# Optimization experiments

Hardware: AMD Instinct MI355X
Metric: run time of the kernel (lower is better)

## Reference

```python
import jax, jax.numpy as jnp
import numpy as np

N = 100_000   # nodes
E = 3_200_000 # edges
K = 3         # num_stacks
T = 4         # num_layers (shared weights)
H = 16        # hidden channels of conv1
EPS = 1e-5    # BatchNorm eps


def setup_inputs() -> dict:
    key = jax.random.key(0)
    ks = jax.random.split(key, 12)
    def glorot(k, shape):
        fan = shape[-2] + shape[-1]
        return jax.random.normal(k, shape, jnp.float32) * (2.0 / fan) ** 0.5
    return {
        "x": jax.random.normal(ks[0], (N, 1), jnp.float32),
        "edge_index": jax.random.randint(ks[1], (2, E), 0, N, jnp.int32),
        "edge_weight": jax.random.uniform(ks[2], (E,), jnp.float32),
        # conv1: in=1, out=16  (init_weight [K,Fin,Fout], shared weight [K,Fout,Fout], root [K,Fin,Fout], bias [K,Fout])
        "conv1_init_w": glorot(ks[3], (K, 1, H)),
        "conv1_w": glorot(ks[4], (K, H, H)),
        "conv1_root_w": glorot(ks[5], (K, 1, H)),
        "conv1_bias": jnp.zeros((K, H), jnp.float32),
        # BatchNorm1d(16) in eval mode: running stats + affine params
        "bn1_gamma": jnp.ones((H,), jnp.float32),
        "bn1_beta": jnp.zeros((H,), jnp.float32),
        "bn1_mean": jnp.zeros((H,), jnp.float32),
        "bn1_var": jnp.ones((H,), jnp.float32),
        # conv2: in=16, out=1, act=None
        "conv2_init_w": glorot(ks[6], (K, H, 1)),
        "conv2_w": glorot(ks[7], (K, 1, 1)),
        "conv2_root_w": glorot(ks[8], (K, H, 1)),
        "conv2_bias": jnp.zeros((K, 1), jnp.float32),
    }


def _gcn_norm(edge_index, edge_weight):
    # ARMAConv uses gcn_norm with add_self_loops=False
    row, col = edge_index[0], edge_index[1]
    deg = jax.ops.segment_sum(edge_weight, col, num_segments=N)
    dis = jnp.where(deg > 0, jax.lax.rsqrt(jnp.maximum(deg, 1e-12)), 0.0)
    norm = dis[row] * edge_weight * dis[col]
    return row, col, norm


def _arma(x, row, col, norm, init_w, w, root_w, bias, act):
    # x: [N, Fin]; out per stack: [K, N, Fout]
    root = jnp.einsum('nf,kfo->kno', x, root_w) + bias[:, None, :]
    out = jnp.einsum('nf,kfo->kno', x, init_w)
    for t in range(T):
        if t > 0:
            out = jnp.einsum('kno,kop->knp', out, w)  # shared weight
        msg = out[:, row, :] * norm[None, :, None]     # [K, E, F] gather + scale
        out = jax.ops.segment_sum(msg.transpose(1, 0, 2), col, num_segments=N)  # [N, K, F]
        out = out.transpose(1, 0, 2) + root            # scatter-add + skip (root)
        if act:
            out = jax.nn.relu(out)
    return out.mean(axis=0)  # mean over stacks -> [N, Fout]


def reference(x, edge_index, edge_weight,
              conv1_init_w, conv1_w, conv1_root_w, conv1_bias,
              bn1_gamma, bn1_beta, bn1_mean, bn1_var,
              conv2_init_w, conv2_w, conv2_root_w, conv2_bias):
    row, col, norm = _gcn_norm(edge_index, edge_weight)
    h = _arma(x, row, col, norm, conv1_init_w, conv1_w, conv1_root_w, conv1_bias, act=True)
    # BatchNorm1d (eval) + ReLU; dropout is identity in eval
    h = (h - bn1_mean) * jax.lax.rsqrt(bn1_var + EPS) * bn1_gamma + bn1_beta
    h = jax.nn.relu(h)
    h = _arma(h, row, col, norm, conv2_init_w, conv2_w, conv2_root_w, conv2_bias, act=False)
    return jax.nn.sigmoid(h)  # [N, 1]
```

## Files before the change

### kernel.cpp

```cpp
#include <hip/hip_runtime.h>
#include <math.h>

#define NN 100000
#define NE 3200000
#define NBUCK 782
#define EPB 4096
#define NBLK 782
#define SB_Q 16
#define SCAP 4608
#define BN_EPS 1e-5f

static inline size_t alignup(size_t v) { return (v + 255) & ~size_t(255); }

__device__ inline unsigned short f2bf(float x) {
  unsigned u = __float_as_uint(x);
  u += 0x7FFF + ((u >> 16) & 1);
  return (unsigned short)(u >> 16);
}
__device__ inline float bf2f(unsigned short h) {
  return __uint_as_float((unsigned)h << 16);
}
__device__ inline float edgew(int e) {
  return __uint_as_float((unsigned)e & 0xFFFE0000u);
}

__global__ void k_hist(const int* __restrict__ col, int* __restrict__ cntm) {
  __shared__ int cnt[NBUCK];
  for (int i = threadIdx.x; i < NBUCK; i += 256) cnt[i] = 0;
  __syncthreads();
  int e0 = blockIdx.x * EPB;
  int nE = min(EPB, NE - e0);
  for (int i = threadIdx.x; i < nE; i += 256) atomicAdd(&cnt[col[e0 + i] >> 7], 1);
  __syncthreads();
  int* dst = cntm + (size_t)blockIdx.x * NBUCK;
  for (int i = threadIdx.x; i < NBUCK; i += 256) dst[i] = cnt[i];
}

__global__ void k_scanb(const int* __restrict__ cntm, int* __restrict__ basem,
                        int* __restrict__ btot) {
  __shared__ int s[NBLK][SB_Q + 1];
  int q0 = blockIdx.x * SB_Q;
  int nq = min(SB_Q, NBUCK - q0);
  int t = threadIdx.x;
  for (int idx = t; idx < NBLK * SB_Q; idx += 256) {
    int i = idx >> 4, j = idx & 15;
    s[i][j] = (j < nq) ? cntm[(size_t)i * NBUCK + q0 + j] : 0;
  }
  __syncthreads();
  int wave = t >> 6, lane = t & 63;
  for (int j = wave; j < SB_Q; j += 4) {
    int carry = 0;
    for (int c = 0; c < (NBLK + 63) / 64; ++c) {
      int i = c * 64 + lane;
      int v = (i < NBLK) ? s[i][j] : 0;
      int x = v;
      #pragma unroll
      for (int d = 1; d < 64; d <<= 1) {
        int tt = __shfl_up(x, d, 64);
        if (lane >= d) x += tt;
      }
      if (i < NBLK) s[i][j] = x - v + carry;
      carry += __shfl(x, 63, 64);
    }
    if (lane == 0 && j < nq) {
      btot[q0 + j] = carry;
      basem[(size_t)NBLK * NBUCK + q0 + j] = carry;
    }
  }
  __syncthreads();
  for (int idx = t; idx < NBLK * SB_Q; idx += 256) {
    int i = idx >> 4, j = idx & 15;
    if (j < nq) basem[(size_t)i * NBUCK + q0 + j] = s[i][j];
  }
}

__global__ void k_scanq(const int* __restrict__ btot, int* __restrict__ gbase) {
  __shared__ int s[NBUCK];
  __shared__ int c[256];
  const int NCH = (NBUCK + 3) / 4;
  int t = threadIdx.x;
  for (int i = t; i < NBUCK; i += 256) s[i] = btot[i];
  __syncthreads();
  if (t < NCH) {
    int b0 = 4 * t, sum = 0;
    #pragma unroll
    for (int j = 0; j < 4; ++j) if (b0 + j < NBUCK) sum += s[b0 + j];
    c[t] = sum;
  }
  __syncthreads();
  for (int d = 1; d < NCH; d <<= 1) {
    int v = (t < NCH && t >= d) ? c[t - d] : 0;
    __syncthreads();
    if (t < NCH) c[t] += v;
    __syncthreads();
  }
  if (t < NCH) {
    int b0 = 4 * t;
    int run = (t > 0) ? c[t - 1] : 0;
    #pragma unroll
    for (int j = 0; j < 4; ++j)
      if (b0 + j < NBUCK) { int v = s[b0 + j]; s[b0 + j] = run; run += v; }
  }
  __syncthreads();
  for (int i = t; i < NBUCK; i += 256) gbase[i] = s[i];
}

__global__ void k_scat(const int* __restrict__ row, const int* __restrict__ col,
                       const float* __restrict__ ew, const int* __restrict__ basem,
                       const int* __restrict__ gbase, int2* __restrict__ bin) {
  __shared__ int segB[NBUCK];
  __shared__ int cnt[NBUCK];
  __shared__ int csc[256];
  __shared__ int2 stage[EPB];
  __shared__ unsigned short qarr[EPB];
  int b = blockIdx.x, t = threadIdx.x;
  const int* rowA = basem + (size_t)b * NBUCK;
  const int* rowB = basem + (size_t)(b + 1) * NBUCK;
  for (int i = t; i < NBUCK; i += 256) {
    int a = rowA[i];
    segB[i] = gbase[i] + a;
    cnt[i] = rowB[i] - a;
  }
  __syncthreads();
  const int NCH = (NBUCK + 3) / 4;
  int q4 = 4 * t;
  if (t < NCH) {
    int sum = 0;
    #pragma unroll
    for (int j = 0; j < 4; ++j) if (q4 + j < NBUCK) sum += cnt[q4 + j];
    csc[t] = sum;
  }
  __syncthreads();
  for (int d = 1; d < NCH; d <<= 1) {
    int v = (t < NCH && t >= d) ? csc[t - d] : 0;
    __syncthreads();
    if (t < NCH) csc[t] += v;
    __syncthreads();
  }
  if (t < NCH) {
    int run = (t > 0) ? csc[t - 1] : 0;
    #pragma unroll
    for (int j = 0; j < 4; ++j)
      if (q4 + j < NBUCK) {
        int v = cnt[q4 + j];
        segB[q4 + j] -= run;
        cnt[q4 + j] = run;
        run += v;
      }
  }
  __syncthreads();
  int e0 = b * EPB;
  int nE = min(EPB, NE - e0);
  for (int i = t; i < nE; i += 256) {
    int e = e0 + i;
    int cc = col[e], q = cc >> 7;
    int p = atomicAdd(&cnt[q], 1);
    stage[p] = make_int2(row[e] | ((cc & 127) << 17), __float_as_int(ew[e]));
    qarr[p] = (unsigned short)q;
  }
  __syncthreads();
  for (int p = t; p < nE; p += 256) {
    int q = qarr[p];
    bin[segB[q] + p] = stage[p];
  }
}

__global__ void k_build(const int* __restrict__ gbase, const int* __restrict__ btot,
                        const int2* __restrict__ bin,
                        int* __restrict__ csr, float* __restrict__ dis,
                        int* __restrict__ nstart, int* __restrict__ ncnt) {
  __shared__ int2 stage[SCAP];
  __shared__ int cnt[128];
  __shared__ float degw[128];
  __shared__ int off[129];
  int b = blockIdx.x;
  int gb0 = gbase[b];
  int nb = btot[b];
  const int2* gb = bin + gb0;
  for (int i = threadIdx.x; i < 128; i += 256) { cnt[i] = 0; degw[i] = 0.f; }
  __syncthreads();
  for (int i = threadIdx.x; i < nb; i += 256) {
    int2 v = gb[i];
    if (i < SCAP) stage[i] = v;
    int c = (v.x >> 17) & 127;
    atomicAdd(&cnt[c], 1);
    atomicAdd(&degw[c], __int_as_float(v.y));
  }
  __syncthreads();
  if (threadIdx.x == 0) {
    int s = 0;
    for (int c = 0; c < 128; ++c) { off[c] = s; s += cnt[c]; }
    off[128] = s;
  }
  __syncthreads();
  for (int c = threadIdx.x; c < 128; c += 256) {
    int n = b * 128 + c;
    if (n < NN) {
      nstart[n] = gb0 + off[c];
      ncnt[n] = cnt[c];
      float d = degw[c];
      dis[n] = (d > 0.f) ? rsqrtf(fmaxf(d, 1e-12f)) : 0.f;
    }
  }
  __syncthreads();
  for (int i = threadIdx.x; i < 128; i += 256) cnt[i] = 0;
  __syncthreads();
  int* cb = csr + gb0;
  for (int i = threadIdx.x; i < nb; i += 256) {
    int2 v = (i < SCAP) ? stage[i] : gb[i];
    int c = (v.x >> 17) & 127;
    int pos = off[c] + atomicAdd(&cnt[c], 1);
    unsigned u = (unsigned)v.y;
    u += 0xFFFFu + ((u >> 17) & 1);
    cb[pos] = (v.x & 0x1FFFF) | (int)(u & 0xFFFE0000u);
  }
}

__global__ void k_init1(const float* __restrict__ x, const float* __restrict__ rw,
                        const float* __restrict__ bias, const float* __restrict__ dis,
                        unsigned short* __restrict__ root1, float* __restrict__ s) {
  int idx = blockIdx.x * 256 + threadIdx.x;
  if (idx >= NN * 16) return;
  int n = idx >> 4, f = idx & 15;
  float xv = x[n];
  if (f == 0) s[n] = dis[n] * xv;
  root1[n * 48 + f]      = f2bf(xv * rw[f]      + bias[f]);
  root1[n * 48 + 16 + f] = f2bf(xv * rw[16 + f] + bias[16 + f]);
  root1[n * 48 + 32 + f] = f2bf(xv * rw[32 + f] + bias[32 + f]);
}

__global__ void k_prop_first(const float* __restrict__ s,
                             const unsigned short* __restrict__ root,
                             ushort4* __restrict__ outp, const int* __restrict__ csr,
                             const int* __restrict__ nstart, const int* __restrict__ ncnt,
                             const float* __restrict__ dis, const float* __restrict__ w,
                             const float* __restrict__ iw) {
  __shared__ float ws[768];
  for (int i = threadIdx.x; i < 768; i += 256) ws[i] = w[i];
  __syncthreads();
  int f = threadIdx.x & 15;
  int n = (blockIdx.x * 256 + threadIdx.x) >> 4;
  if (n >= NN) return;
  int e0 = nstart[n], cnt = ncnt[n];
  float g = 0.f;
  for (int i = f; i < cnt; i += 16) {
    int e = csr[e0 + i];
    g = fmaf(edgew(e), s[e & 0x1FFFF], g);
  }
  #pragma unroll
  for (int d = 8; d; d >>= 1) g += __shfl_xor(g, d, 16);
  float dn = dis[n];
  float dg = dn * g;
  float a0 = fmaxf(fmaf(dg, iw[f],      bf2f(root[n * 48 + f])),      0.f);
  float a1 = fmaxf(fmaf(dg, iw[16 + f], bf2f(root[n * 48 + 16 + f])), 0.f);
  float a2 = fmaxf(fmaf(dg, iw[32 + f], bf2f(root[n * 48 + 32 + f])), 0.f);
  float n0 = 0.f, n1 = 0.f, n2 = 0.f;
  #pragma unroll
  for (int f2 = 0; f2 < 16; ++f2) {
    float b0 = __shfl(a0, f2, 16);
    float b1 = __shfl(a1, f2, 16);
    float b2v = __shfl(a2, f2, 16);
    n0 = fmaf(b0, ws[f2 * 16 + f], n0);
    n1 = fmaf(b1, ws[256 + f2 * 16 + f], n1);
    n2 = fmaf(b2v, ws[512 + f2 * 16 + f], n2);
  }
  ushort4 pk;
  pk.x = f2bf(dn * n0); pk.y = f2bf(dn * n1); pk.z = f2bf(dn * n2); pk.w = 0;
  outp[(size_t)n * 16 + f] = pk;
}

template <bool APPLY_W>
__global__ __launch_bounds__(256, 6)
void k_prop16(const ushort4* __restrict__ in,
              const unsigned short* __restrict__ root,
              ushort4* __restrict__ outp, const int* __restrict__ csr,
              const int* __restrict__ nstart, const int* __restrict__ ncnt,
              const float* __restrict__ dis, const float* __restrict__ w,
              const float* __restrict__ bng, const float* __restrict__ bnb,
              const float* __restrict__ bnm, const float* __restrict__ bnv,
              const float* __restrict__ iw2, const float* __restrict__ rw2,
              const float* __restrict__ b2,
              float4* __restrict__ root2, ushort4* __restrict__ o2) {
  __shared__ float ws[768];
  if (APPLY_W) {
    for (int i = threadIdx.x; i < 768; i += 256) ws[i] = w[i];
    __syncthreads();
  }
  int f = threadIdx.x & 15;
  int n = (blockIdx.x * 256 + threadIdx.x) >> 4;
  if (n >= NN) return;
  int e0 = nstart[n], cnt = ncnt[n];
  float a0 = 0.f, a1 = 0.f, a2 = 0.f;
  int i = 0;
  for (; i + 16 <= cnt; i += 16) {
    int e[16];
    ushort4 v[16];
    #pragma unroll
    for (int j = 0; j < 16; ++j) e[j] = csr[e0 + i + j];
    #pragma unroll
    for (int j = 0; j < 16; ++j) v[j] = in[(size_t)(e[j] & 0x1FFFF) * 16 + f];
    #pragma unroll
    for (int j = 0; j < 16; ++j) {
      float we = edgew(e[j]);
      a0 = fmaf(we, bf2f(v[j].x), a0);
      a1 = fmaf(we, bf2f(v[j].y), a1);
      a2 = fmaf(we, bf2f(v[j].z), a2);
    }
  }
  for (; i + 4 <= cnt; i += 4) {
    int e[4];
    ushort4 v[4];
    #pragma unroll
    for (int j = 0; j < 4; ++j) e[j] = csr[e0 + i + j];
    #pragma unroll
    for (int j = 0; j < 4; ++j) v[j] = in[(size_t)(e[j] & 0x1FFFF) * 16 + f];
    #pragma unroll
    for (int j = 0; j < 4; ++j) {
      float we = edgew(e[j]);
      a0 = fmaf(we, bf2f(v[j].x), a0);
      a1 = fmaf(we, bf2f(v[j].y), a1);
      a2 = fmaf(we, bf2f(v[j].z), a2);
    }
  }
  for (; i < cnt; ++i) {
    int e = csr[e0 + i];
    float we = edgew(e);
    ushort4 v = in[(size_t)(e & 0x1FFFF) * 16 + f];
    a0 = fmaf(we, bf2f(v.x), a0);
    a1 = fmaf(we, bf2f(v.y), a1);
    a2 = fmaf(we, bf2f(v.z), a2);
  }
  float dn = dis[n];
  a0 = fmaxf(fmaf(dn, a0, bf2f(root[n * 48 + f])),      0.f);
  a1 = fmaxf(fmaf(dn, a1, bf2f(root[n * 48 + 16 + f])), 0.f);
  a2 = fmaxf(fmaf(dn, a2, bf2f(root[n * 48 + 32 + f])), 0.f);
  if (APPLY_W) {
    float n0 = 0.f, n1 = 0.f, n2 = 0.f;
    #pragma unroll
    for (int f2 = 0; f2 < 16; ++f2) {
      float b0 = __shfl(a0, f2, 16);
      float b1 = __shfl(a1, f2, 16);
      float b2v = __shfl(a2, f2, 16);
      n0 = fmaf(b0, ws[f2 * 16 + f], n0);
      n1 = fmaf(b1, ws[256 + f2 * 16 + f], n1);
      n2 = fmaf(b2v, ws[512 + f2 * 16 + f], n2);
    }
    ushort4 pk;
    pk.x = f2bf(dn * n0); pk.y = f2bf(dn * n1); pk.z = f2bf(dn * n2); pk.w = 0;
    outp[(size_t)n * 16 + f] = pk;
  } else {
    float mean = (a0 + a1 + a2) * (1.f / 3.f);
    float hv = fmaxf((mean - bnm[f]) * rsqrtf(bnv[f] + BN_EPS) * bng[f] + bnb[f], 0.f);
    float d0 = hv * iw2[f],      r0 = hv * rw2[f];
    float d1 = hv * iw2[16 + f], r1 = hv * rw2[16 + f];
    float d2 = hv * iw2[32 + f], r2 = hv * rw2[32 + f];
    #pragma unroll
    for (int d = 8; d; d >>= 1) {
      d0 += __shfl_xor(d0, d, 16); r0 += __shfl_xor(r0, d, 16);
      d1 += __shfl_xor(d1, d, 16); r1 += __shfl_xor(r1, d, 16);
      d2 += __shfl_xor(d2, d, 16); r2 += __shfl_xor(r2, d, 16);
    }
    if (f == 0) {
      float4 rt;
      rt.x = r0 + b2[0]; rt.y = r1 + b2[1]; rt.z = r2 + b2[2]; rt.w = 0.f;
      root2[n] = rt;
      ushort4 pk;
      pk.x = f2bf(dn * d0); pk.y = f2bf(dn * d1); pk.z = f2bf(dn * d2); pk.w = 0;
      o2[n] = pk;
    }
  }
}

template <bool LAST>
__global__ void k_prop1(const ushort4* __restrict__ in, const float4* __restrict__ root,
                        ushort4* __restrict__ outp, float* __restrict__ outf,
                        const int* __restrict__ csr,
                        const int* __restrict__ nstart, const int* __restrict__ ncnt,
                        const float* __restrict__ dis, const float* __restrict__ w2) {
  int lane = threadIdx.x & 15;
  int n = (blockIdx.x * 256 + threadIdx.x) >> 4;
  if (n >= NN) return;
  int e0 = nstart[n], cnt = ncnt[n];
  float a0 = 0.f, a1 = 0.f, a2 = 0.f;
  for (int i = lane; i < cnt; i += 16) {
    int e = csr[e0 + i];
    float we = edgew(e);
    ushort4 src = in[e & 0x1FFFF];
    a0 = fmaf(we, bf2f(src.x), a0);
    a1 = fmaf(we, bf2f(src.y), a1);
    a2 = fmaf(we, bf2f(src.z), a2);
  }
  #pragma unroll
  for (int d = 8; d; d >>= 1) {
    a0 += __shfl_xor(a0, d, 16);
    a1 += __shfl_xor(a1, d, 16);
    a2 += __shfl_xor(a2, d, 16);
  }
  if (lane == 0) {
    float dn = dis[n];
    float4 rt = root[n];
    if (LAST) {
      float s = fmaf(dn, a0, rt.x) + fmaf(dn, a1, rt.y) + fmaf(dn, a2, rt.z);
      s *= (1.f / 3.f);
      outf[n] = 1.f / (1.f + expf(-s));
    } else {
      ushort4 pk;
      pk.x = f2bf(dn * fmaf(dn, a0, rt.x) * w2[0]);
      pk.y = f2bf(dn * fmaf(dn, a1, rt.y) * w2[1]);
      pk.z = f2bf(dn * fmaf(dn, a2, rt.z) * w2[2]);
      pk.w = 0;
      outp[n] = pk;
    }
  }
}

extern "C" void kernel_launch(void* const* d_in, const int* in_sizes, int n_in,
                              void* d_out, int out_size, void* d_ws, size_t ws_size,
                              hipStream_t stream) {
  const float* x     = (const float*)d_in[0];
  const int*   ei    = (const int*)d_in[1];
  const float* ew    = (const float*)d_in[2];
  const float* c1_iw = (const float*)d_in[3];
  const float* c1_w  = (const float*)d_in[4];
  const float* c1_rw = (const float*)d_in[5];
  const float* c1_b  = (const float*)d_in[6];
  const float* bn_g  = (const float*)d_in[7];
  const float* bn_b  = (const float*)d_in[8];
  const float* bn_m  = (const float*)d_in[9];
  const float* bn_v  = (const float*)d_in[10];
  const float* c2_iw = (const float*)d_in[11];
  const float* c2_w  = (const float*)d_in[12];
  const float* c2_rw = (const float*)d_in[13];
  const float* c2_b  = (const float*)d_in[14];
  float* out = (float*)d_out;

  char* p = (char*)d_ws;
  auto take = [&](size_t bytes) -> char* { char* r = p; p += alignup(bytes); return r; };
  int*     cntm   = (int*)take((size_t)NBLK * NBUCK * 4);
  int*     basem  = (int*)take((size_t)(NBLK + 1) * NBUCK * 4);
  int*     btot   = (int*)take((size_t)NBUCK * 4);
  int*     gbase  = (int*)take((size_t)NBUCK * 4);
  int2*    bin    = (int2*)take((size_t)NE * 8);
  int*     csr    = (int*)take((size_t)NE * 4);
  float*   dis    = (float*)take((size_t)NN * 4);
  int*     nst    = (int*)take((size_t)NN * 4);
  int*     ncn    = (int*)take((size_t)NN * 4);
  unsigned short* root1 = (unsigned short*)take((size_t)NN * 48 * 2);
  float*   sbuf   = (float*)take((size_t)NN * 4);
  ushort4* bufA   = (ushort4*)take((size_t)NN * 16 * 8);
  ushort4* bufB   = (ushort4*)take((size_t)NN * 16 * 8);
  float4*  root2  = (float4*)take((size_t)NN * 16);
  ushort4* o2A    = (ushort4*)take((size_t)NN * 8);
  ushort4* o2B    = (ushort4*)take((size_t)NN * 8);

  const int* row = ei;
  const int* col = ei + NE;

  const int gP = (NN * 16 + 255) / 256;
  const int gSB = (NBUCK + SB_Q - 1) / SB_Q;

  k_hist <<<NBLK, 256, 0, stream>>>(col, cntm);
  k_scanb<<<gSB, 256, 0, stream>>>(cntm, basem, btot);
  k_scanq<<<1, 256, 0, stream>>>(btot, gbase);
  k_scat <<<NBLK, 256, 0, stream>>>(row, col, ew, basem, gbase, bin);
  k_build<<<NBUCK, 256, 0, stream>>>(gbase, btot, bin, csr, dis, nst, ncn);

  k_init1<<<gP, 256, 0, stream>>>(x, c1_rw, c1_b, dis, root1, sbuf);
  k_prop_first<<<gP, 256, 0, stream>>>(sbuf, root1, bufA, csr, nst, ncn, dis, c1_w, c1_iw);
  k_prop16<true ><<<gP, 256, 0, stream>>>(bufA, root1, bufB, csr, nst, ncn, dis, c1_w,
      nullptr, nullptr, nullptr, nullptr, nullptr, nullptr, nullptr, nullptr, nullptr);
  k_prop16<true ><<<gP, 256, 0, stream>>>(bufB, root1, bufA, csr, nst, ncn, dis, c1_w,
      nullptr, nullptr, nullptr, nullptr, nullptr, nullptr, nullptr, nullptr, nullptr);
  k_prop16<false><<<gP, 256, 0, stream>>>(bufA, root1, nullptr, csr, nst, ncn, dis, nullptr,
      bn_g, bn_b, bn_m, bn_v, c2_iw, c2_rw, c2_b, root2, o2A);

  k_prop1<false><<<gP, 256, 0, stream>>>(o2A, root2, o2B, nullptr, csr, nst, ncn, dis, c2_w);
  k_prop1<false><<<gP, 256, 0, stream>>>(o2B, root2, o2A, nullptr, csr, nst, ncn, dis, c2_w);
  k_prop1<false><<<gP, 256, 0, stream>>>(o2A, root2, o2B, nullptr, csr, nst, ncn, dis, c2_w);
  k_prop1<true ><<<gP, 256, 0, stream>>>(o2B, root2, nullptr, out, csr, nst, ncn, dis, c2_w);
}
```

Baseline: 383.5 us.

## Sort nodes by in-degree within each bucket to balance wavefront work

k_build now counting-sorts the 128 nodes of each bucket by in-degree and writes a permutation array. Every propagation kernel maps its thread group to perm[gid], so nodes with similar degree share a wavefront and lanes diverge less in loop trip counts. The k_prop16 edge unroll also drops from 16 to 8 and the launch_bounds occupancy hint is removed. The cost is an extra indirection per node and less spatial locality in the per-node loads and stores.

```diff
diff --git a/kernel.cpp b/kernel.cpp
--- a/kernel.cpp
+++ b/kernel.cpp
@@ -168,16 +168,19 @@
 __global__ void k_build(const int* __restrict__ gbase, const int* __restrict__ btot,
                         const int2* __restrict__ bin,
                         int* __restrict__ csr, float* __restrict__ dis,
-                        int* __restrict__ nstart, int* __restrict__ ncnt) {
+                        int* __restrict__ nstart, int* __restrict__ ncnt,
+                        int* __restrict__ perm) {
   __shared__ int2 stage[SCAP];
   __shared__ int cnt[128];
   __shared__ float degw[128];
   __shared__ int off[129];
+  __shared__ int dh[129];
   int b = blockIdx.x;
   int gb0 = gbase[b];
   int nb = btot[b];
   const int2* gb = bin + gb0;
   for (int i = threadIdx.x; i < 128; i += 256) { cnt[i] = 0; degw[i] = 0.f; }
+  for (int i = threadIdx.x; i < 129; i += 256) dh[i] = 0;
   __syncthreads();
   for (int i = threadIdx.x; i < nb; i += 256) {
     int2 v = gb[i];
@@ -200,6 +203,19 @@
       ncnt[n] = cnt[c];
       float d = degw[c];
       dis[n] = (d > 0.f) ? rsqrtf(fmaxf(d, 1e-12f)) : 0.f;
+      atomicAdd(&dh[min(cnt[c], 127) + 1], 1);
+    }
+  }
+  __syncthreads();
+  if (threadIdx.x == 0) {
+    for (int d = 1; d < 129; ++d) dh[d] += dh[d - 1];
+  }
+  __syncthreads();
+  for (int c = threadIdx.x; c < 128; c += 256) {
+    int n = b * 128 + c;
+    if (n < NN) {
+      int r = atomicAdd(&dh[min(cnt[c], 127)], 1);
+      perm[b * 128 + r] = n;
     }
   }
   __syncthreads();
@@ -234,13 +250,14 @@
                              ushort4* __restrict__ outp, const int* __restrict__ csr,
                              const int* __restrict__ nstart, const int* __restrict__ ncnt,
                              const float* __restrict__ dis, const float* __restrict__ w,
-                             const float* __restrict__ iw) {
+                             const float* __restrict__ iw, const int* __restrict__ perm) {
   __shared__ float ws[768];
   for (int i = threadIdx.x; i < 768; i += 256) ws[i] = w[i];
   __syncthreads();
   int f = threadIdx.x & 15;
-  int n = (blockIdx.x * 256 + threadIdx.x) >> 4;
-  if (n >= NN) return;
+  int gid = (blockIdx.x * 256 + threadIdx.x) >> 4;
+  if (gid >= NN) return;
+  int n = perm[gid];
   int e0 = nstart[n], cnt = ncnt[n];
   float g = 0.f;
   for (int i = f; i < cnt; i += 16) {
@@ -270,37 +287,38 @@
 }
 
 template <bool APPLY_W>
-__global__ __launch_bounds__(256, 6)
-void k_prop16(const ushort4* __restrict__ in,
-              const unsigned short* __restrict__ root,
-              ushort4* __restrict__ outp, const int* __restrict__ csr,
-              const int* __restrict__ nstart, const int* __restrict__ ncnt,
-              const float* __restrict__ dis, const float* __restrict__ w,
-              const float* __restrict__ bng, const float* __restrict__ bnb,
-              const float* __restrict__ bnm, const float* __restrict__ bnv,
-              const float* __restrict__ iw2, const float* __restrict__ rw2,
-              const float* __restrict__ b2,
-              float4* __restrict__ root2, ushort4* __restrict__ o2) {
+__global__ void k_prop16(const ushort4* __restrict__ in,
+                         const unsigned short* __restrict__ root,
+                         ushort4* __restrict__ outp, const int* __restrict__ csr,
+                         const int* __restrict__ nstart, const int* __restrict__ ncnt,
+                         const float* __restrict__ dis, const float* __restrict__ w,
+                         const float* __restrict__ bng, const float* __restrict__ bnb,
+                         const float* __restrict__ bnm, const float* __restrict__ bnv,
+                         const float* __restrict__ iw2, const float* __restrict__ rw2,
+                         const float* __restrict__ b2,
+                         float4* __restrict__ root2, ushort4* __restrict__ o2,
+                         const int* __restrict__ perm) {
   __shared__ float ws[768];
   if (APPLY_W) {
     for (int i = threadIdx.x; i < 768; i += 256) ws[i] = w[i];
     __syncthreads();
   }
   int f = threadIdx.x & 15;
-  int n = (blockIdx.x * 256 + threadIdx.x) >> 4;
-  if (n >= NN) return;
+  int gid = (blockIdx.x * 256 + threadIdx.x) >> 4;
+  if (gid >= NN) return;
+  int n = perm[gid];
   int e0 = nstart[n], cnt = ncnt[n];
   float a0 = 0.f, a1 = 0.f, a2 = 0.f;
   int i = 0;
-  for (; i + 16 <= cnt; i += 16) {
-    int e[16];
-    ushort4 v[16];
-    #pragma unroll
-    for (int j = 0; j < 16; ++j) e[j] = csr[e0 + i + j];
-    #pragma unroll
-    for (int j = 0; j < 16; ++j) v[j] = in[(size_t)(e[j] & 0x1FFFF) * 16 + f];
-    #pragma unroll
-    for (int j = 0; j < 16; ++j) {
+  for (; i + 8 <= cnt; i += 8) {
+    int e[8];
+    ushort4 v[8];
+    #pragma unroll
+    for (int j = 0; j < 8; ++j) e[j] = csr[e0 + i + j];
+    #pragma unroll
+    for (int j = 0; j < 8; ++j) v[j] = in[(size_t)(e[j] & 0x1FFFF) * 16 + f];
+    #pragma unroll
+    for (int j = 0; j < 8; ++j) {
       float we = edgew(e[j]);
       a0 = fmaf(we, bf2f(v[j].x), a0);
       a1 = fmaf(we, bf2f(v[j].y), a1);
@@ -376,10 +394,12 @@
                         ushort4* __restrict__ outp, float* __restrict__ outf,
                         const int* __restrict__ csr,
                         const int* __restrict__ nstart, const int* __restrict__ ncnt,
-                        const float* __restrict__ dis, const float* __restrict__ w2) {
+                        const float* __restrict__ dis, const float* __restrict__ w2,
+                        const int* __restrict__ perm) {
   int lane = threadIdx.x & 15;
-  int n = (blockIdx.x * 256 + threadIdx.x) >> 4;
-  if (n >= NN) return;
+  int gid = (blockIdx.x * 256 + threadIdx.x) >> 4;
+  if (gid >= NN) return;
+  int n = perm[gid];
   int e0 = nstart[n], cnt = ncnt[n];
   float a0 = 0.f, a1 = 0.f, a2 = 0.f;
   for (int i = lane; i < cnt; i += 16) {
@@ -445,6 +465,7 @@
   float*   dis    = (float*)take((size_t)NN * 4);
   int*     nst    = (int*)take((size_t)NN * 4);
   int*     ncn    = (int*)take((size_t)NN * 4);
+  int*     perm   = (int*)take((size_t)NN * 4);
   unsigned short* root1 = (unsigned short*)take((size_t)NN * 48 * 2);
   float*   sbuf   = (float*)take((size_t)NN * 4);
   ushort4* bufA   = (ushort4*)take((size_t)NN * 16 * 8);
@@ -463,19 +484,19 @@
   k_scanb<<<gSB, 256, 0, stream>>>(cntm, basem, btot);
   k_scanq<<<1, 256, 0, stream>>>(btot, gbase);
   k_scat <<<NBLK, 256, 0, stream>>>(row, col, ew, basem, gbase, bin);
-  k_build<<<NBUCK, 256, 0, stream>>>(gbase, btot, bin, csr, dis, nst, ncn);
+  k_build<<<NBUCK, 256, 0, stream>>>(gbase, btot, bin, csr, dis, nst, ncn, perm);
 
   k_init1<<<gP, 256, 0, stream>>>(x, c1_rw, c1_b, dis, root1, sbuf);
-  k_prop_first<<<gP, 256, 0, stream>>>(sbuf, root1, bufA, csr, nst, ncn, dis, c1_w, c1_iw);
+  k_prop_first<<<gP, 256, 0, stream>>>(sbuf, root1, bufA, csr, nst, ncn, dis, c1_w, c1_iw, perm);
   k_prop16<true ><<<gP, 256, 0, stream>>>(bufA, root1, bufB, csr, nst, ncn, dis, c1_w,
-      nullptr, nullptr, nullptr, nullptr, nullptr, nullptr, nullptr, nullptr, nullptr);
+      nullptr, nullptr, nullptr, nullptr, nullptr, nullptr, nullptr, nullptr, nullptr, perm);
   k_prop16<true ><<<gP, 256, 0, stream>>>(bufB, root1, bufA, csr, nst, ncn, dis, c1_w,
-      nullptr, nullptr, nullptr, nullptr, nullptr, nullptr, nullptr, nullptr, nullptr);
+      nullptr, nullptr, nullptr, nullptr, nullptr, nullptr, nullptr, nullptr, nullptr, perm);
   k_prop16<false><<<gP, 256, 0, stream>>>(bufA, root1, nullptr, csr, nst, ncn, dis, nullptr,
-      bn_g, bn_b, bn_m, bn_v, c2_iw, c2_rw, c2_b, root2, o2A);
-
-  k_prop1<false><<<gP, 256, 0, stream>>>(o2A, root2, o2B, nullptr, csr, nst, ncn, dis, c2_w);
-  k_prop1<false><<<gP, 256, 0, stream>>>(o2B, root2, o2A, nullptr, csr, nst, ncn, dis, c2_w);
-  k_prop1<false><<<gP, 256, 0, stream>>>(o2A, root2, o2B, nullptr, csr, nst, ncn, dis, c2_w);
-  k_prop1<true ><<<gP, 256, 0, stream>>>(o2B, root2, nullptr, out, csr, nst, ncn, dis, c2_w);
-}
+      bn_g, bn_b, bn_m, bn_v, c2_iw, c2_rw, c2_b, root2, o2A, perm);
+
+  k_prop1<false><<<gP, 256, 0, stream>>>(o2A, root2, o2B, nullptr, csr, nst, ncn, dis, c2_w, perm);
+  k_prop1<false><<<gP, 256, 0, stream>>>(o2B, root2, o2A, nullptr, csr, nst, ncn, dis, c2_w, perm);
+  k_prop1<false><<<gP, 256, 0, stream>>>(o2A, root2, o2B, nullptr, csr, nst, ncn, dis, c2_w, perm);
+  k_prop1<true ><<<gP, 256, 0, stream>>>(o2B, root2, nullptr, out, csr, nst, ncn, dis, c2_w, perm);
+}
```

After: 443.3 us. 15.6% more time.
